# Kernel tuning notes

Hardware: AMD Instinct MI355X
Metric: run time of the kernel (lower is better)

## Reference

```python
import jax, jax.numpy as jnp
import numpy as np

BITS = 8
EPS = 1e-08


def _scalar_quantize_maxabs(x, scale, bits, eps):
    # clamp(round(x / scale), -qmax, qmax) with a fixed (precomputed) scalar scale
    qmax = float(2 ** (bits - 1) - 1)
    s = jnp.maximum(scale, eps)
    return jnp.clip(jnp.round(x / s), -qmax, qmax)


def setup_inputs() -> dict:
    key = jax.random.key(0)
    k1, k2, k3 = jax.random.split(key, 3)
    B, S, D_in, D_out = 4, 2048, 2048, 2048
    hidden_states = jax.random.normal(k1, (B, S, D_in), dtype=jnp.float32)
    # weight_quantized holds low-bit integer values stored as float (as produced by the quantizer)
    qmax = float(2 ** (BITS - 1) - 1)
    weight_quantized = jnp.round(
        jnp.clip(jax.random.normal(k2, (D_in, D_out), dtype=jnp.float32) * (qmax / 3.0), -qmax, qmax)
    )
    x_scale = jnp.asarray(0.05, dtype=jnp.float32)
    bias = jax.random.normal(k3, (D_out,), dtype=jnp.float32)
    return {
        "hidden_states": hidden_states,
        "weight_quantized": weight_quantized,
        "x_scale": x_scale,
        "bias": bias,
    }


def reference(hidden_states, weight_quantized, x_scale, bias) -> jnp.ndarray:
    original_shape = hidden_states.shape[:-1]
    input_dim = hidden_states.shape[-1]
    x_flat = hidden_states.reshape(-1, input_dim)  # [B*S, D_in]
    x_q = _scalar_quantize_maxabs(x_flat, x_scale.reshape(()), BITS, EPS)
    out = x_q.astype(weight_quantized.dtype) @ weight_quantized  # [B*S, D_out]
    out = out + bias.astype(out.dtype)[None, :]
    return out.astype(hidden_states.dtype).reshape(*original_shape, weight_quantized.shape[1])
```

## Files before the change

### kernel.cpp

```cpp
#include <hip/hip_runtime.h>
#include <cstdint>
#include <cstddef>

#define MDIM 8192
#define NDIM 2048
#define KDIM 2048

constexpr int BM = 128, BN = 256, BK = 64;

typedef int v4i __attribute__((ext_vector_type(4)));

__device__ __forceinline__ void async_ld16(const void* g, void* l) {
    __builtin_amdgcn_global_load_lds(
        (const __attribute__((address_space(1))) int*)g,
        (__attribute__((address_space(3))) int*)l,
        16, 0, 0);
}

__device__ __forceinline__ uint32_t q8(float x, float inv) {
    float q = fminf(fmaxf(rintf(x * inv), -127.f), 127.f);
    return (uint32_t)((int)q) & 0xffu;
}

#define WBLOCKS ((KDIM / 64) * (NDIM / 64))
#define XCHUNK (MDIM * KDIM / 4 / 4)
#define XBLOCKS (XCHUNK / 256)

__global__ void quant_kernel(const float4* __restrict__ x, uint32_t* __restrict__ xq,
                             const float* __restrict__ scale_p,
                             const float* __restrict__ w, uint32_t* __restrict__ wt) {
    __shared__ uint32_t t[64][17];
    const int tid = threadIdx.x;

    if (blockIdx.x >= WBLOCKS) {
        int i = (blockIdx.x - WBLOCKS) * 256 + tid;
        float inv = 1.0f / fmaxf(scale_p[0], 1e-8f);
#pragma unroll
        for (int k = 0; k < 4; ++k) {
            float4 v = x[i + k * XCHUNK];
            xq[i + k * XCHUNK] =
                q8(v.x, inv) | (q8(v.y, inv) << 8) | (q8(v.z, inv) << 16) | (q8(v.w, inv) << 24);
        }
        return;
    }

    const int bid = blockIdx.x;
    const int k0 = (bid >> 5) * 64;
    const int n0 = (bid & 31) * 64;
    const int rr  = tid >> 4;
    const int c4  = (tid & 15) * 4;
#pragma unroll
    for (int p = 0; p < 4; ++p) {
        int r = rr + p * 16;
        float4 v = *(const float4*)&w[(size_t)(k0 + r) * NDIM + n0 + c4];
        uint32_t pk = (uint32_t)((int)rintf(v.x) & 0xff)
                    | ((uint32_t)((int)rintf(v.y) & 0xff) << 8)
                    | ((uint32_t)((int)rintf(v.z) & 0xff) << 16)
                    | ((uint32_t)((int)rintf(v.w) & 0xff) << 24);
        t[r][c4 >> 2] = pk;
    }
    __syncthreads();
#pragma unroll
    for (int p = 0; p < 4; ++p) {
        int c = rr + p * 16;
        uint32_t o = 0;
#pragma unroll
        for (int j = 0; j < 4; ++j) {
            uint32_t b = (t[c4 + j][c >> 2] >> ((c & 3) * 8)) & 0xffu;
            o |= b << (j * 8);
        }
        wt[((size_t)(n0 + c) * KDIM + k0 + c4) >> 2] = o;
    }
}

__global__ __launch_bounds__(512, 4)
void gemm_i8_kernel(const int8_t* __restrict__ A,
                    const int8_t* __restrict__ Bt,
                    const float* __restrict__ bias,
                    float* __restrict__ C) {
    __shared__ alignas(16) int8_t lA[2][BM * BK];
    __shared__ alignas(16) int8_t lB[2][BN * BK];

    const int tid  = threadIdx.x;
    const int lane = tid & 63;
    const int wave = tid >> 6;
    const int wm   = wave & 1;
    const int wn   = wave >> 1;

    const int bidlin = blockIdx.y * gridDim.x + blockIdx.x;
    const int xcd    = bidlin & 7;
    const int idx    = bidlin >> 3;
    const int m0     = (xcd * 8 + (idx >> 3)) * BM;
    const int n0     = (idx & 7) * BN;

    const int srow = lane >> 2;
    const int schk = (lane & 3) ^ ((srow >> 1) & 3);
    const int8_t* gA = A  + (size_t)(m0 + wave * 16 + srow) * KDIM + schk * 16;
    const int8_t* gB = Bt + (size_t)(n0 + wave * 32 + srow) * KDIM + schk * 16;
    const int lwoA = wave * 1024;
    const int lwoB = wave * 2048;

    const int quad = lane >> 4;
    const int lr   = lane & 15;
    const int fchk = (quad ^ ((lr >> 1) & 3)) * 16;
    const int aoff = (wm * 64 + lr) * BK + fchk;
    const int boff = (wn * 64 + lr) * BK + fchk;

    v4i acc[4][4];
#pragma unroll
    for (int i = 0; i < 4; ++i)
#pragma unroll
        for (int j = 0; j < 4; ++j)
            acc[i][j] = (v4i){0, 0, 0, 0};

#define STAGE(buf, kof)                                                        \
    do {                                                                       \
        async_ld16(gA + (kof), &lA[buf][lwoA]);                                \
        async_ld16(gB + (kof), &lB[buf][lwoB]);                                \
        async_ld16(gB + (kof) + (size_t)16 * KDIM, &lB[buf][lwoB + 1024]);     \
    } while (0)

#define COMPUTE(buf)                                                           \
    do {                                                                       \
        v4i af[4], bf[4];                                                      \
        _Pragma("unroll")                                                      \
        for (int i = 0; i < 4; ++i)                                            \
            af[i] = *(const v4i*)&lA[buf][aoff + i * 1024];                    \
        _Pragma("unroll")                                                      \
        for (int j = 0; j < 4; ++j)                                            \
            bf[j] = *(const v4i*)&lB[buf][boff + j * 1024];                    \
        _Pragma("unroll")                                                      \
        for (int i = 0; i < 4; ++i)                                            \
            _Pragma("unroll")                                                  \
            for (int j = 0; j < 4; ++j)                                        \
                acc[i][j] = __builtin_amdgcn_mfma_i32_16x16x64_i8(             \
                    af[i], bf[j], acc[i][j], 0, 0, 0);                         \
    } while (0)

    STAGE(0, 0);
    int kof = BK;
    for (int it = 0; it < KDIM / BK - 1; ++it) {
        __syncthreads();
        STAGE((it + 1) & 1, kof);
        kof += BK;
        COMPUTE(it & 1);
    }
    __syncthreads();
    COMPUTE((KDIM / BK - 1) & 1);

    const int crow = m0 + wm * 64 + quad * 4;
    const int ccol = n0 + wn * 64 + lr;
    float bj[4];
#pragma unroll
    for (int j = 0; j < 4; ++j) bj[j] = bias[ccol + j * 16];
#pragma unroll
    for (int i = 0; i < 4; ++i)
#pragma unroll
        for (int j = 0; j < 4; ++j)
#pragma unroll
            for (int r = 0; r < 4; ++r)
                C[(size_t)(crow + i * 16 + r) * NDIM + (ccol + j * 16)] = (float)acc[i][j][r] + bj[j];
}

extern "C" void kernel_launch(void* const* d_in, const int* in_sizes, int n_in,
                              void* d_out, int out_size, void* d_ws, size_t ws_size,
                              hipStream_t stream) {
    const float* x    = (const float*)d_in[0];
    const float* w    = (const float*)d_in[1];
    const float* xs   = (const float*)d_in[2];
    const float* bias = (const float*)d_in[3];
    float* out = (float*)d_out;

    int8_t* xq = (int8_t*)d_ws;
    int8_t* wt = xq + (size_t)MDIM * KDIM;

    quant_kernel<<<WBLOCKS + XBLOCKS, 256, 0, stream>>>(
        (const float4*)x, (uint32_t*)xq, xs, w, (uint32_t*)wt);
    gemm_i8_kernel<<<dim3(NDIM / BN, MDIM / BM), 512, 0, stream>>>(xq, wt, bias, out);
}
```

Measured before the change: 163.9 us.

## Fuse activation quantization into GEMM A-tile loading

Drops the separate activation quantize pass and its int8 workspace round trip. The GEMM now loads fp32 activations straight into registers, quantizes them to int8 and writes the packed tile into LDS, overlapping the global load with the MFMA work of the previous buffer. The cost is that each A tile is re-read as fp32 by every N-block (8 column blocks), which is 4x the A bytes per tile. It also adds register pressure and VALU work inside the main loop.

```diff
diff --git a/kernel.cpp b/kernel.cpp
--- a/kernel.cpp
+++ b/kernel.cpp
@@ -21,29 +21,13 @@
     float q = fminf(fmaxf(rintf(x * inv), -127.f), 127.f);
     return (uint32_t)((int)q) & 0xffu;
 }
+__device__ __forceinline__ uint32_t q8x4(float4 v, float inv) {
+    return q8(v.x, inv) | (q8(v.y, inv) << 8) | (q8(v.z, inv) << 16) | (q8(v.w, inv) << 24);
+}
 
-#define WBLOCKS ((KDIM / 64) * (NDIM / 64))
-#define XCHUNK (MDIM * KDIM / 4 / 4)
-#define XBLOCKS (XCHUNK / 256)
-
-__global__ void quant_kernel(const float4* __restrict__ x, uint32_t* __restrict__ xq,
-                             const float* __restrict__ scale_p,
-                             const float* __restrict__ w, uint32_t* __restrict__ wt) {
+__global__ void quant_w_kernel(const float* __restrict__ w, uint32_t* __restrict__ wt) {
     __shared__ uint32_t t[64][17];
     const int tid = threadIdx.x;
-
-    if (blockIdx.x >= WBLOCKS) {
-        int i = (blockIdx.x - WBLOCKS) * 256 + tid;
-        float inv = 1.0f / fmaxf(scale_p[0], 1e-8f);
-#pragma unroll
-        for (int k = 0; k < 4; ++k) {
-            float4 v = x[i + k * XCHUNK];
-            xq[i + k * XCHUNK] =
-                q8(v.x, inv) | (q8(v.y, inv) << 8) | (q8(v.z, inv) << 16) | (q8(v.w, inv) << 24);
-        }
-        return;
-    }
-
     const int bid = blockIdx.x;
     const int k0 = (bid >> 5) * 64;
     const int n0 = (bid & 31) * 64;
@@ -74,8 +58,9 @@
 }
 
 __global__ __launch_bounds__(512, 4)
-void gemm_i8_kernel(const int8_t* __restrict__ A,
+void gemm_i8_kernel(const float* __restrict__ X,
                     const int8_t* __restrict__ Bt,
+                    const float* __restrict__ scale_p,
                     const float* __restrict__ bias,
                     float* __restrict__ C) {
     __shared__ alignas(16) int8_t lA[2][BM * BK];
@@ -95,7 +80,7 @@
 
     const int srow = lane >> 2;
     const int schk = (lane & 3) ^ ((srow >> 1) & 3);
-    const int8_t* gA = A  + (size_t)(m0 + wave * 16 + srow) * KDIM + schk * 16;
+    const float*  gA = X  + (size_t)(m0 + wave * 16 + srow) * KDIM + schk * 16;
     const int8_t* gB = Bt + (size_t)(n0 + wave * 32 + srow) * KDIM + schk * 16;
     const int lwoA = wave * 1024;
     const int lwoB = wave * 2048;
@@ -106,6 +91,8 @@
     const int aoff = (wm * 64 + lr) * BK + fchk;
     const int boff = (wn * 64 + lr) * BK + fchk;
 
+    const float inv = 1.0f / fmaxf(scale_p[0], 1e-8f);
+
     v4i acc[4][4];
 #pragma unroll
     for (int i = 0; i < 4; ++i)
@@ -113,40 +100,63 @@
         for (int j = 0; j < 4; ++j)
             acc[i][j] = (v4i){0, 0, 0, 0};
 
-#define STAGE(buf, kof)                                                        \
+    float4 a0, a1, a2, a3;
+
+#define A_LOAD(kof)                                                            \
     do {                                                                       \
-        async_ld16(gA + (kof), &lA[buf][lwoA]);                                \
+        const float4* p = (const float4*)(gA + (kof));                         \
+        a0 = p[0]; a1 = p[1]; a2 = p[2]; a3 = p[3];                            \
+    } while (0)
+
+#define A_WRITE(buf)                                                           \
+    do {                                                                       \
+        v4i pk = { (int)q8x4(a0, inv), (int)q8x4(a1, inv),                     \
+                   (int)q8x4(a2, inv), (int)q8x4(a3, inv) };                   \
+        *(v4i*)&lA[buf][lwoA + lane * 16] = pk;                                \
+    } while (0)
+
+#define STAGE_B(buf, kof)                                                      \
+    do {                                                                       \
         async_ld16(gB + (kof), &lB[buf][lwoB]);                                \
         async_ld16(gB + (kof) + (size_t)16 * KDIM, &lB[buf][lwoB + 1024]);     \
     } while (0)
 
 #define COMPUTE(buf)                                                           \
     do {                                                                       \
-        v4i af[4], bf[4];                                                      \
-        _Pragma("unroll")                                                      \
-        for (int i = 0; i < 4; ++i)                                            \
-            af[i] = *(const v4i*)&lA[buf][aoff + i * 1024];                    \
+        v4i bf[4];                                                             \
         _Pragma("unroll")                                                      \
         for (int j = 0; j < 4; ++j)                                            \
             bf[j] = *(const v4i*)&lB[buf][boff + j * 1024];                    \
         _Pragma("unroll")                                                      \
-        for (int i = 0; i < 4; ++i)                                            \
+        for (int i = 0; i < 4; ++i) {                                          \
+            v4i af = *(const v4i*)&lA[buf][aoff + i * 1024];                   \
             _Pragma("unroll")                                                  \
             for (int j = 0; j < 4; ++j)                                        \
                 acc[i][j] = __builtin_amdgcn_mfma_i32_16x16x64_i8(             \
-                    af[i], bf[j], acc[i][j], 0, 0, 0);                         \
+                    af, bf[j], acc[i][j], 0, 0, 0);                            \
+        }                                                                      \
     } while (0)
 
-    STAGE(0, 0);
+    A_LOAD(0);
+    STAGE_B(0, 0);
+    A_WRITE(0);
     int kof = BK;
     for (int it = 0; it < KDIM / BK - 1; ++it) {
         __syncthreads();
-        STAGE((it + 1) & 1, kof);
+        A_LOAD(kof);
+        STAGE_B((it + 1) & 1, kof);
+        asm volatile("" ::: "memory");
+        COMPUTE(it & 1);
+        A_WRITE((it + 1) & 1);
         kof += BK;
-        COMPUTE(it & 1);
     }
     __syncthreads();
     COMPUTE((KDIM / BK - 1) & 1);
+
+#undef A_LOAD
+#undef A_WRITE
+#undef STAGE_B
+#undef COMPUTE
 
     const int crow = m0 + wm * 64 + quad * 4;
     const int ccol = n0 + wn * 64 + lr;
@@ -171,10 +181,8 @@
     const float* bias = (const float*)d_in[3];
     float* out = (float*)d_out;
 
-    int8_t* xq = (int8_t*)d_ws;
-    int8_t* wt = xq + (size_t)MDIM * KDIM;
+    int8_t* wt = (int8_t*)d_ws;
 
-    quant_kernel<<<WBLOCKS + XBLOCKS, 256, 0, stream>>>(
-        (const float4*)x, (uint32_t*)xq, xs, w, (uint32_t*)wt);
-    gemm_i8_kernel<<<dim3(NDIM / BN, MDIM / BM), 512, 0, stream>>>(xq, wt, bias, out);
+    quant_w_kernel<<<(KDIM / 64) * (NDIM / 64), 256, 0, stream>>>(w, (uint32_t*)wt);
+    gemm_i8_kernel<<<dim3(NDIM / BN, MDIM / BM), 512, 0, stream>>>(x, wt, xs, bias, out);
 }
```

Measured after the change: 195.6 us. 1.19x slower.
